# Kernel tuning notes

Measured on AMD Instinct MI355X. Metric: run time of the kernel, lower is better.

Reference implementation:

```python
import jax, jax.numpy as jnp
import numpy as np

N = 65536      # nodes in batched graph
E = 2097152    # edges (avg degree 32)
V = 1000       # chord vocabulary size
F_IN = 128     # chord feature dim
H = 256        # hidden_dim
OUT = 128      # out_dim
G = 256        # number of graphs in batch


def _gcn_layer(x, W, b, row, col, norm, n):
    # x: [n, f_in] -> [n, f_out]; PyG GCNConv: linear then normalized aggregation + bias
    x = x @ W
    msg = x[row] * norm[:, None]            # gather at source, scale by sym-norm
    return jax.ops.segment_sum(msg, col, num_segments=n) + b


def setup_inputs() -> dict:
    key = jax.random.key(0)
    ks = jax.random.split(key, 9)
    chord_feats = jax.random.normal(ks[0], (V, F_IN), jnp.float32)
    W1 = jax.random.normal(ks[1], (F_IN, H), jnp.float32) * 0.05
    b1 = jnp.zeros((H,), jnp.float32)
    W2 = jax.random.normal(ks[2], (H, OUT), jnp.float32) * 0.05
    b2 = jnp.zeros((OUT,), jnp.float32)
    edge_attr = jax.random.uniform(ks[3], (E,), jnp.float32)          # positive edge weights
    node_indices = jax.random.randint(ks[4], (N,), 0, V, jnp.int64)
    edge_index = jax.random.randint(ks[5], (2, E), 0, N, jnp.int64)
    batch_index = jnp.sort(jax.random.randint(ks[6], (N,), 0, G, jnp.int64))
    return {"chord_feats": chord_feats, "W1": W1, "b1": b1, "W2": W2, "b2": b2,
            "edge_attr": edge_attr, "node_indices": node_indices,
            "edge_index": edge_index, "batch_index": batch_index}


def reference(chord_feats, W1, b1, W2, b2, edge_attr, node_indices, edge_index, batch_index):
    loops = jnp.arange(N, dtype=edge_index.dtype)
    row = jnp.concatenate([edge_index[0], loops])   # source
    col = jnp.concatenate([edge_index[1], loops])   # target
    ew = jnp.concatenate([edge_attr, jnp.ones((N,), edge_attr.dtype)])  # self-loop weight 1
    # symmetric GCN normalization: D^-1/2 A D^-1/2
    deg = jax.ops.segment_sum(ew, col, num_segments=N)
    dis = jnp.where(deg > 0, jax.lax.rsqrt(jnp.maximum(deg, 1e-30)), 0.0)
    norm = dis[row] * ew * dis[col]

    x = chord_feats[node_indices]                   # [N, F_IN]
    x = jax.nn.relu(_gcn_layer(x, W1, b1, row, col, norm, N))
    x = jax.nn.relu(_gcn_layer(x, W2, b2, row, col, norm, N))

    # global_mean_pool over batch_index
    sums = jax.ops.segment_sum(x, batch_index, num_segments=G)
    counts = jax.ops.segment_sum(jnp.ones((N,), x.dtype), batch_index, num_segments=G)
    return sums / jnp.maximum(counts, 1.0)[:, None]
```

## Files before the change

kernel.cpp:

```cpp
#include <hip/hip_runtime.h>
#include <hip/hip_fp16.h>
#include <math.h>

constexpr int N_NODES = 65536;
constexpr int N_EDGES = 2097152;
constexpr int F_IN    = 128;
constexpr int H_DIM   = 256;
constexpr int O_DIM   = 128;
constexpr int N_GRAPH = 256;
constexpr int V_SIZE  = 1000;

constexpr int EPB  = 8192;
constexpr int NBLK = N_EDGES / EPB;
constexpr float FXP = 16777216.0f;

typedef _Float16 half8 __attribute__((ext_vector_type(8)));
typedef float floatx4 __attribute__((ext_vector_type(4)));


__global__ void k_init(float* __restrict__ pool, const int* __restrict__ batch,
                       float* __restrict__ cntf, const float* __restrict__ cf,
                       const float* __restrict__ W1, __half* __restrict__ cfW1,
                       const float* __restrict__ W2, _Float16* __restrict__ W2T) {
    __shared__ float xs[8 * F_IN];
    int i = blockIdx.x * blockDim.x + threadIdx.x;
    if (i < N_GRAPH * O_DIM) pool[i] = 0.0f;
    if (blockIdx.x == 0) {
        int g = threadIdx.x;
        int lo = 0, hi = N_NODES;
        while (lo < hi) { int m = (lo + hi) >> 1; if (batch[m] < g) lo = m + 1; else hi = m; }
        int start = lo;
        lo = 0; hi = N_NODES;
        while (lo < hi) { int m = (lo + hi) >> 1; if (batch[m] <= g) lo = m + 1; else hi = m; }
        cntf[g] = (float)(lo - start);
    }
    if (blockIdx.x < V_SIZE / 8) {
        int rb = blockIdx.x * 8;
        int t  = threadIdx.x;
        #pragma unroll
        for (int p = 0; p < 4; ++p) {
            int idx = p * 256 + t;
            int r = idx >> 7, k = idx & 127;
            xs[idx] = cf[(size_t)(rb + r) * F_IN + k];
        }
        __syncthreads();
        float acc[8] = {};
        for (int k = 0; k < F_IN; ++k) {
            float w = W1[k * H_DIM + t];
            #pragma unroll
            for (int j = 0; j < 8; ++j) acc[j] += xs[j * F_IN + k] * w;
        }
        #pragma unroll
        for (int j = 0; j < 8; ++j)
            cfW1[(size_t)(rb + j) * H_DIM + t] = __float2half(acc[j]);
    }
    if (blockIdx.x >= 128) {
        int idx = (blockIdx.x - 128) * 256 + threadIdx.x;
        int nn = idx >> 8, kk = idx & 255;
        W2T[idx] = (_Float16)W2[kk * O_DIM + nn];
    }
}


__global__ void k_hist(const int* __restrict__ col, int* __restrict__ hist) {
    __shared__ int h[256];
    int t = threadIdx.x;
    h[t] = 0;
    __syncthreads();
    int base = blockIdx.x * EPB;
    #pragma unroll
    for (int i = 0; i < EPB / 256; ++i)
        atomicAdd(&h[col[base + i * 256 + t] >> 8], 1);
    __syncthreads();
    hist[t * NBLK + blockIdx.x] = h[t];
}


__global__ void k_scan1(const int* __restrict__ in, int* __restrict__ out,
                        int* __restrict__ bsum) {
    __shared__ int s[256];
    int tid = threadIdx.x;
    int i = blockIdx.x * 256 + tid;
    int v = in[i];
    s[tid] = v;
    __syncthreads();
    for (int d = 1; d < 256; d <<= 1) {
        int t = (tid >= d) ? s[tid - d] : 0;
        __syncthreads();
        s[tid] += t;
        __syncthreads();
    }
    out[i] = s[tid] - v;
    if (tid == 255) bsum[blockIdx.x] = s[255];
}

__global__ void k_scan2(int* __restrict__ bsum) {
    __shared__ int s[256];
    int tid = threadIdx.x;
    int v = bsum[tid];
    s[tid] = v;
    __syncthreads();
    for (int d = 1; d < 256; d <<= 1) {
        int t = (tid >= d) ? s[tid - d] : 0;
        __syncthreads();
        s[tid] += t;
        __syncthreads();
    }
    bsum[tid] = s[tid] - v;
}


__global__ void k_part(const int* __restrict__ row, const int* __restrict__ col,
                       const float* __restrict__ ew, const int* __restrict__ nidx,
                       const int* __restrict__ hoffs, const int* __restrict__ bsum,
                       int2* __restrict__ part) {
    __shared__ int cur[256];
    int t = threadIdx.x;
    cur[t] = hoffs[t * NBLK + blockIdx.x] + bsum[t];
    __syncthreads();
    int base = blockIdx.x * EPB;
    for (int i = 0; i < EPB / 256; ++i) {
        int e = base + i * 256 + t;
        int r = row[e], c = col[e];
        unsigned hw = (unsigned)__half_as_ushort(__float2half(ew[e]));
        int vb = nidx[r];
        int slot = atomicAdd(&cur[c >> 8], 1);
        int2 rec;
        rec.x = (r << 16) | ((c & 255) << 8) | (vb >> 2);
        rec.y = (int)(((unsigned)(vb & 3) << 16) | hw);
        part[slot] = rec;
    }
}


__global__ void k_build1(const int* __restrict__ hoffs, const int* __restrict__ bsum,
                         const int2* __restrict__ part, float* __restrict__ dis,
                         int* __restrict__ offs) {
    __shared__ unsigned long long dc[256];
    __shared__ int sc[256];
    int t = threadIdx.x;
    int bucket = blockIdx.x;
    dc[t] = 0ULL;
    __syncthreads();
    int start = hoffs[bucket * NBLK] + bsum[bucket];
    int end   = (bucket == 255) ? N_EDGES : (hoffs[(bucket + 1) * NBLK] + bsum[bucket + 1]);
    for (int j = start + t; j < end; j += 256) {
        int2 rec = part[j];
        int dst = (rec.x >> 8) & 255;
        float w = __half2float(__ushort_as_half((unsigned short)(rec.y & 0xFFFF)));
        atomicAdd(&dc[dst], (1ULL << 40) |
                  (unsigned long long)(unsigned)(w * FXP + 0.5f));
    }
    __syncthreads();
    unsigned long long v = dc[t];
    float deg = 1.0f + (float)(v & 0xFFFFFFFFFFULL) * (1.0f / FXP);
    dis[bucket * 256 + t] = 1.0f / sqrtf(deg);
    int cnt = (int)(v >> 40);
    sc[t] = cnt;
    __syncthreads();
    for (int d = 1; d < 256; d <<= 1) {
        int x = (t >= d) ? sc[t - d] : 0;
        __syncthreads();
        sc[t] += x;
        __syncthreads();
    }
    offs[bucket * 256 + t] = start + sc[t] - cnt;
    if (bucket == 255 && t == 255) offs[N_NODES] = N_EDGES;
}


__global__ void k_build2(const int* __restrict__ hoffs, const int* __restrict__ bsum,
                         const int2* __restrict__ part, const float* __restrict__ dis,
                         const int* __restrict__ offs, int2* __restrict__ csr) {
    __shared__ int cur[256];
    int t = threadIdx.x;
    int bucket = blockIdx.x;
    cur[t] = offs[bucket * 256 + t];
    __syncthreads();
    int start = hoffs[bucket * NBLK] + bsum[bucket];
    int end   = (bucket == 255) ? N_EDGES : (hoffs[(bucket + 1) * NBLK] + bsum[bucket + 1]);
    for (int j = start + t; j < end; j += 256) {
        int2 rec = part[j];
        int dst = (rec.x >> 8) & 255;
        unsigned src = ((unsigned)rec.x) >> 16;
        int vb = ((rec.x & 255) << 2) | ((rec.y >> 16) & 3);
        float w = __half2float(__ushort_as_half((unsigned short)(rec.y & 0xFFFF)));
        float nm = dis[src] * w;
        int slot = atomicAdd(&cur[dst], 1);
        int2 e;
        e.x = (int)((src << 10) | (unsigned)vb);
        e.y = __float_as_int(nm);
        csr[slot] = e;
    }
}


__global__ void k_agg1(const int2* __restrict__ cfW1, const int* __restrict__ nidx,
                       const float* __restrict__ dis, const int* __restrict__ offs,
                       const int2* __restrict__ csr, const float4* __restrict__ b1f4,
                       int2* __restrict__ h1) {
    int wave = threadIdx.x >> 6;
    int lane = threadIdx.x & 63;
    int c = blockIdx.x * 4 + wave;
    float d = dis[c];
    int2 sp = cfW1[(size_t)nidx[c] * 64 + lane];
    float2 sa = __half22float2(*(__half2*)&sp.x);
    float2 sb = __half22float2(*(__half2*)&sp.y);
    float4 esum = {0.f, 0.f, 0.f, 0.f};
    int a0 = offs[c], a1 = offs[c + 1];
    int s = a0;
    for (; s + 8 <= a1; s += 8) {
        int sb_i = __builtin_amdgcn_readfirstlane(s);
        int2 e[8];
        #pragma unroll
        for (int u = 0; u < 8; ++u) e[u] = csr[sb_i + u];
        int2 v[8];
        #pragma unroll
        for (int u = 0; u < 8; ++u)
            v[u] = cfW1[(size_t)(e[u].x & 1023) * 64 + lane];
        #pragma unroll
        for (int u = 0; u < 8; ++u) {
            float n = __int_as_float(e[u].y);
            float2 va = __half22float2(*(__half2*)&v[u].x);
            float2 vb = __half22float2(*(__half2*)&v[u].y);
            esum.x += va.x * n; esum.y += va.y * n;
            esum.z += vb.x * n; esum.w += vb.y * n;
        }
    }
    for (; s < a1; ++s) {
        int sb_i = __builtin_amdgcn_readfirstlane(s);
        int2 e0 = csr[sb_i];
        int2 v0 = cfW1[(size_t)(e0.x & 1023) * 64 + lane];
        float n = __int_as_float(e0.y);
        float2 va = __half22float2(*(__half2*)&v0.x);
        float2 vb = __half22float2(*(__half2*)&v0.y);
        esum.x += va.x * n; esum.y += va.y * n;
        esum.z += vb.x * n; esum.w += vb.y * n;
    }
    float4 bb = b1f4[lane];
    float dd = d * d;
    float r0 = bb.x + sa.x * dd + d * esum.x;
    float r1 = bb.y + sa.y * dd + d * esum.y;
    float r2 = bb.z + sb.x * dd + d * esum.z;
    float r3 = bb.w + sb.y * dd + d * esum.w;
    r0 = r0 > 0.f ? r0 : 0.f;  r1 = r1 > 0.f ? r1 : 0.f;
    r2 = r2 > 0.f ? r2 : 0.f;  r3 = r3 > 0.f ? r3 : 0.f;
    float2 p0 = {r0, r1}, p1 = {r2, r3};
    __half2 ha = __float22half2_rn(p0);
    __half2 hb = __float22half2_rn(p1);
    int2 outv;
    outv.x = *(int*)&ha;
    outv.y = *(int*)&hb;
    h1[(size_t)c * 64 + lane] = outv;
}


__global__ void k_gemm2(const _Float16* __restrict__ h1, const _Float16* __restrict__ W2T,
                        __half* __restrict__ xw2h) {
    int wave = threadIdx.x >> 6;
    int lane = threadIdx.x & 63;
    int quad = lane >> 4;
    int n    = lane & 15;
    int tm   = blockIdx.x * 4 + wave;
    const _Float16* arow = h1 + (size_t)(tm * 16 + n) * H_DIM;
    half8 a[8];
    #pragma unroll
    for (int kt = 0; kt < 8; ++kt)
        a[kt] = *(const half8*)(arow + kt * 32 + quad * 8);
    #pragma unroll
    for (int nt = 0; nt < 8; ++nt) {
        floatx4 acc = {0.f, 0.f, 0.f, 0.f};
        const _Float16* brow = W2T + (size_t)(nt * 16 + n) * H_DIM;
        #pragma unroll
        for (int kt = 0; kt < 8; ++kt) {
            half8 b = *(const half8*)(brow + kt * 32 + quad * 8);
            acc = __builtin_amdgcn_mfma_f32_16x16x32_f16(a[kt], b, acc, 0, 0, 0);
        }
        #pragma unroll
        for (int r = 0; r < 4; ++r) {
            int rowi = tm * 16 + quad * 4 + r;
            xw2h[(size_t)rowi * O_DIM + nt * 16 + n] = __float2half(acc[r]);
        }
    }
}


__global__ void k_agg2_pool(const __half2* __restrict__ xw2h, const float* __restrict__ b2,
                            const float* __restrict__ dis, const int* __restrict__ offs,
                            const int2* __restrict__ csr, const int* __restrict__ batch,
                            float* __restrict__ pool) {
    __shared__ float2 red[4][64];
    __shared__ int bgs[4];
    int wave = threadIdx.x >> 6;
    int lane = threadIdx.x & 63;
    int c = blockIdx.x * 4 + wave;
    float d = dis[c];
    float2 self = __half22float2(xw2h[(size_t)c * 64 + lane]);
    float2 bb = ((const float2*)b2)[lane];
    float2 esum = {0.f, 0.f};
    int s0 = offs[c], s1 = offs[c + 1];
    int s = s0;
    for (; s + 8 <= s1; s += 8) {
        int sb_i = __builtin_amdgcn_readfirstlane(s);
        int2 e[8];
        #pragma unroll
        for (int u = 0; u < 8; ++u) e[u] = csr[sb_i + u];
        float2 v[8];
        #pragma unroll
        for (int u = 0; u < 8; ++u)
            v[u] = __half22float2(xw2h[(size_t)(e[u].x >> 10) * 64 + lane]);
        #pragma unroll
        for (int u = 0; u < 8; ++u) {
            float n = __int_as_float(e[u].y);
            esum.x += v[u].x * n; esum.y += v[u].y * n;
        }
    }
    for (; s < s1; ++s) {
        int sb_i = __builtin_amdgcn_readfirstlane(s);
        int2 e0 = csr[sb_i];
        float2 v0 = __half22float2(xw2h[(size_t)(e0.x >> 10) * 64 + lane]);
        float n0 = __int_as_float(e0.y);
        esum.x += v0.x * n0; esum.y += v0.y * n0;
    }
    float dd = d * d;
    float2 acc;
    acc.x = bb.x + self.x * dd + d * esum.x;
    acc.y = bb.y + self.y * dd + d * esum.y;
    acc.x = acc.x > 0.0f ? acc.x : 0.0f;
    acc.y = acc.y > 0.0f ? acc.y : 0.0f;
    red[wave][lane] = acc;
    if (lane == 0) bgs[wave] = batch[c];
    __syncthreads();
    if (wave == 0) {
        float2 a = red[0][lane];
        int cg = bgs[0];
        #pragma unroll
        for (int w = 1; w < 4; ++w) {
            int g = bgs[w];
            float2 r = red[w][lane];
            if (g == cg) { a.x += r.x; a.y += r.y; }
            else {
                atomicAdd(&pool[cg * O_DIM + 2 * lane], a.x);
                atomicAdd(&pool[cg * O_DIM + 2 * lane + 1], a.y);
                a = r; cg = g;
            }
        }
        atomicAdd(&pool[cg * O_DIM + 2 * lane], a.x);
        atomicAdd(&pool[cg * O_DIM + 2 * lane + 1], a.y);
    }
}

__global__ void k_final(const float* __restrict__ pool, const float* __restrict__ cnt,
                        float* __restrict__ out) {
    int t = blockIdx.x * blockDim.x + threadIdx.x;
    if (t < N_GRAPH * O_DIM) {
        int g = t / O_DIM;
        out[t] = pool[t] / fmaxf(cnt[g], 1.0f);
    }
}


extern "C" void kernel_launch(void* const* d_in, const int* in_sizes, int n_in,
                              void* d_out, int out_size, void* d_ws, size_t ws_size,
                              hipStream_t stream) {
    const float* cf   = (const float*)d_in[0];
    const float* W1   = (const float*)d_in[1];
    const float* b1   = (const float*)d_in[2];
    const float* W2   = (const float*)d_in[3];
    const float* b2   = (const float*)d_in[4];
    const float* ew   = (const float*)d_in[5];
    const int*   nidx = (const int*)d_in[6];
    const int*   eidx = (const int*)d_in[7];
    const int*   bidx = (const int*)d_in[8];
    float* out = (float*)d_out;

    const int* row = eidx;
    const int* col = eidx + N_EDGES;

    char* ws = (char*)d_ws;
    size_t off = 0;
    int*   hist  = (int*)  (ws + off); off += (size_t)N_NODES * 4;
    int*   hoffs = (int*)  (ws + off); off += (size_t)N_NODES * 4;
    int*   bsum  = (int*)  (ws + off); off += 4096;
    float* dis   = (float*)(ws + off); off += (size_t)N_NODES * 4;
    int*   offs  = (int*)  (ws + off); off += (size_t)(N_NODES + 16) * 4;
    int2*  csr   = (int2*) (ws + off); off += (size_t)N_EDGES * 8;
    float* pool  = (float*)(ws + off); off += (size_t)(N_GRAPH * O_DIM + N_GRAPH) * 4;
    __half* cfW1 = (__half*)(ws + off); off += (size_t)V_SIZE * H_DIM * 2;
    _Float16* W2T = (_Float16*)(ws + off); off += (size_t)O_DIM * H_DIM * 2;
    off = (off + 255) & ~(size_t)255;
    int2*  part  = (int2*) (ws + off); off += (size_t)N_EDGES * 8;
    __half* h1   = (__half*)(ws + off);
    __half* xw2h = (__half*)part;
    float* cntf  = pool + N_GRAPH * O_DIM;

    k_init<<<256, 256, 0, stream>>>(pool, bidx, cntf, cf, W1, cfW1, W2, W2T);
    k_hist<<<NBLK, 256, 0, stream>>>(col, hist);
    k_scan1<<<256, 256, 0, stream>>>(hist, hoffs, bsum);
    k_scan2<<<1, 256, 0, stream>>>(bsum);

    k_part<<<NBLK, 256, 0, stream>>>(row, col, ew, nidx, hoffs, bsum, part);
    k_build1<<<256, 256, 0, stream>>>(hoffs, bsum, part, dis, offs);
    k_build2<<<256, 256, 0, stream>>>(hoffs, bsum, part, dis, offs, csr);

    k_agg1<<<N_NODES / 4, 256, 0, stream>>>((const int2*)cfW1, nidx, dis, offs, csr,
                                            (const float4*)b1, (int2*)h1);

    k_gemm2<<<N_NODES / 64, 256, 0, stream>>>((const _Float16*)h1, W2T, xw2h);
    k_agg2_pool<<<N_NODES / 4, 256, 0, stream>>>((const __half2*)xw2h, b2, dis, offs, csr,
                                                 bidx, pool);

    k_final<<<(N_GRAPH * O_DIM + 255) / 256, 256, 0, stream>>>(pool, cntf, out);
}
```

Before: 348.7 us.

## Widen gathers to 16-byte loads and split each wave across multiple edges

Both aggregation kernels now have each lane gather 8 halves (int4) instead of 2 or 4, so one wave covers a feature row with 16 or 32 lanes and processes several edges at once. Partial sums are combined with cross-lane xor shuffles before the bias, ReLU and store. The goal is fewer, wider memory transactions per gathered row and more edges in flight per wave, cutting load instruction count in these latency-bound gather loops. It adds shuffle reductions and tail handling (odd-start alignment, padded lanes) that idle lanes on low-degree nodes.

```diff
diff --git a/kernel.cpp b/kernel.cpp
--- a/kernel.cpp
+++ b/kernel.cpp
@@ -194,64 +194,103 @@
     }
 }
 
-
-__global__ void k_agg1(const int2* __restrict__ cfW1, const int* __restrict__ nidx,
+__device__ __forceinline__ void acc8(float* e, int4 v, float n) {
+    float2 f0 = __half22float2(*(__half2*)&v.x);
+    float2 f1 = __half22float2(*(__half2*)&v.y);
+    float2 f2 = __half22float2(*(__half2*)&v.z);
+    float2 f3 = __half22float2(*(__half2*)&v.w);
+    e[0] += f0.x * n; e[1] += f0.y * n;
+    e[2] += f1.x * n; e[3] += f1.y * n;
+    e[4] += f2.x * n; e[5] += f2.y * n;
+    e[6] += f3.x * n; e[7] += f3.y * n;
+}
+
+
+__global__ void k_agg1(const int4* __restrict__ cfW1, const int* __restrict__ nidx,
                        const float* __restrict__ dis, const int* __restrict__ offs,
                        const int2* __restrict__ csr, const float4* __restrict__ b1f4,
-                       int2* __restrict__ h1) {
+                       int4* __restrict__ h1) {
     int wave = threadIdx.x >> 6;
     int lane = threadIdx.x & 63;
+    int g    = lane >> 5;
+    int sl   = lane & 31;
     int c = blockIdx.x * 4 + wave;
     float d = dis[c];
-    int2 sp = cfW1[(size_t)nidx[c] * 64 + lane];
-    float2 sa = __half22float2(*(__half2*)&sp.x);
-    float2 sb = __half22float2(*(__half2*)&sp.y);
-    float4 esum = {0.f, 0.f, 0.f, 0.f};
+    int4 sp = cfW1[(size_t)nidx[c] * 32 + sl];
+    float esum[8] = {0.f, 0.f, 0.f, 0.f, 0.f, 0.f, 0.f, 0.f};
     int a0 = offs[c], a1 = offs[c + 1];
     int s = a0;
+    if (s < a1 && (s & 1)) {
+        int sb = __builtin_amdgcn_readfirstlane(s);
+        int2 e0 = csr[sb];
+        int4 v0 = cfW1[(size_t)(e0.x & 1023) * 32 + sl];
+        float n = (g == 0) ? __int_as_float(e0.y) : 0.0f;
+        acc8(esum, v0, n);
+        ++s;
+    }
     for (; s + 8 <= a1; s += 8) {
-        int sb_i = __builtin_amdgcn_readfirstlane(s);
-        int2 e[8];
-        #pragma unroll
-        for (int u = 0; u < 8; ++u) e[u] = csr[sb_i + u];
-        int2 v[8];
-        #pragma unroll
-        for (int u = 0; u < 8; ++u)
-            v[u] = cfW1[(size_t)(e[u].x & 1023) * 64 + lane];
-        #pragma unroll
-        for (int u = 0; u < 8; ++u) {
-            float n = __int_as_float(e[u].y);
-            float2 va = __half22float2(*(__half2*)&v[u].x);
-            float2 vb = __half22float2(*(__half2*)&v[u].y);
-            esum.x += va.x * n; esum.y += va.y * n;
-            esum.z += vb.x * n; esum.w += vb.y * n;
-        }
-    }
-    for (; s < a1; ++s) {
-        int sb_i = __builtin_amdgcn_readfirstlane(s);
-        int2 e0 = csr[sb_i];
-        int2 v0 = cfW1[(size_t)(e0.x & 1023) * 64 + lane];
-        float n = __int_as_float(e0.y);
-        float2 va = __half22float2(*(__half2*)&v0.x);
-        float2 vb = __half22float2(*(__half2*)&v0.y);
-        esum.x += va.x * n; esum.y += va.y * n;
-        esum.z += vb.x * n; esum.w += vb.y * n;
-    }
-    float4 bb = b1f4[lane];
+        int sb = __builtin_amdgcn_readfirstlane(s);
+        int4 ee[4];
+        #pragma unroll
+        for (int u = 0; u < 4; ++u) ee[u] = *(const int4*)(csr + sb + 2 * u);
+        int4 v[4]; float n[4];
+        #pragma unroll
+        for (int u = 0; u < 4; ++u) {
+            int ex = g ? ee[u].z : ee[u].x;
+            int ey = g ? ee[u].w : ee[u].y;
+            n[u] = __int_as_float(ey);
+            v[u] = cfW1[(size_t)(ex & 1023) * 32 + sl];
+        }
+        #pragma unroll
+        for (int u = 0; u < 4; ++u) acc8(esum, v[u], n[u]);
+    }
+    for (; s + 2 <= a1; s += 2) {
+        int sb = __builtin_amdgcn_readfirstlane(s);
+        int4 ee = *(const int4*)(csr + sb);
+        int ex = g ? ee.z : ee.x;
+        int ey = g ? ee.w : ee.y;
+        int4 v0 = cfW1[(size_t)(ex & 1023) * 32 + sl];
+        acc8(esum, v0, __int_as_float(ey));
+    }
+    if (s < a1) {
+        int sb = __builtin_amdgcn_readfirstlane(s);
+        int2 e0 = csr[sb];
+        int4 v0 = cfW1[(size_t)(e0.x & 1023) * 32 + sl];
+        float n = (g == 0) ? __int_as_float(e0.y) : 0.0f;
+        acc8(esum, v0, n);
+    }
+    #pragma unroll
+    for (int k = 0; k < 8; ++k) esum[k] += __shfl_xor(esum[k], 32, 64);
+
     float dd = d * d;
-    float r0 = bb.x + sa.x * dd + d * esum.x;
-    float r1 = bb.y + sa.y * dd + d * esum.y;
-    float r2 = bb.z + sb.x * dd + d * esum.z;
-    float r3 = bb.w + sb.y * dd + d * esum.w;
-    r0 = r0 > 0.f ? r0 : 0.f;  r1 = r1 > 0.f ? r1 : 0.f;
-    r2 = r2 > 0.f ? r2 : 0.f;  r3 = r3 > 0.f ? r3 : 0.f;
-    float2 p0 = {r0, r1}, p1 = {r2, r3};
-    __half2 ha = __float22half2_rn(p0);
-    __half2 hb = __float22half2_rn(p1);
-    int2 outv;
-    outv.x = *(int*)&ha;
-    outv.y = *(int*)&hb;
-    h1[(size_t)c * 64 + lane] = outv;
+    float2 s0 = __half22float2(*(__half2*)&sp.x);
+    float2 s1 = __half22float2(*(__half2*)&sp.y);
+    float2 s2 = __half22float2(*(__half2*)&sp.z);
+    float2 s3 = __half22float2(*(__half2*)&sp.w);
+    float4 bb0 = b1f4[2 * sl];
+    float4 bb1 = b1f4[2 * sl + 1];
+    float r[8];
+    r[0] = bb0.x + s0.x * dd + d * esum[0];
+    r[1] = bb0.y + s0.y * dd + d * esum[1];
+    r[2] = bb0.z + s1.x * dd + d * esum[2];
+    r[3] = bb0.w + s1.y * dd + d * esum[3];
+    r[4] = bb1.x + s2.x * dd + d * esum[4];
+    r[5] = bb1.y + s2.y * dd + d * esum[5];
+    r[6] = bb1.z + s3.x * dd + d * esum[6];
+    r[7] = bb1.w + s3.y * dd + d * esum[7];
+    #pragma unroll
+    for (int k = 0; k < 8; ++k) r[k] = r[k] > 0.f ? r[k] : 0.f;
+    float2 p0 = {r[0], r[1]}, p1 = {r[2], r[3]}, p2 = {r[4], r[5]}, p3 = {r[6], r[7]};
+    __half2 h0 = __float22half2_rn(p0);
+    __half2 h1v = __float22half2_rn(p1);
+    __half2 h2 = __float22half2_rn(p2);
+    __half2 h3 = __float22half2_rn(p3);
+    int4 outv;
+    outv.x = *(int*)&h0;
+    outv.y = *(int*)&h1v;
+    outv.z = *(int*)&h2;
+    outv.w = *(int*)&h3;
+    if (lane < 32) h1[(size_t)c * 32 + sl] = outv;
 }
 
 
@@ -285,59 +324,89 @@
 }
 
 
-__global__ void k_agg2_pool(const __half2* __restrict__ xw2h, const float* __restrict__ b2,
+__global__ void k_agg2_pool(const int4* __restrict__ xw2h, const float* __restrict__ b2,
                             const float* __restrict__ dis, const int* __restrict__ offs,
                             const int2* __restrict__ csr, const int* __restrict__ batch,
                             float* __restrict__ pool) {
-    __shared__ float2 red[4][64];
+    __shared__ float red[4][128];
     __shared__ int bgs[4];
     int wave = threadIdx.x >> 6;
     int lane = threadIdx.x & 63;
+    int grp  = lane >> 4;
+    int sl   = lane & 15;
     int c = blockIdx.x * 4 + wave;
     float d = dis[c];
-    float2 self = __half22float2(xw2h[(size_t)c * 64 + lane]);
-    float2 bb = ((const float2*)b2)[lane];
-    float2 esum = {0.f, 0.f};
+    int4 sp = xw2h[(size_t)c * 16 + sl];
+    float esum[8] = {0.f, 0.f, 0.f, 0.f, 0.f, 0.f, 0.f, 0.f};
     int s0 = offs[c], s1 = offs[c + 1];
     int s = s0;
-    for (; s + 8 <= s1; s += 8) {
-        int sb_i = __builtin_amdgcn_readfirstlane(s);
-        int2 e[8];
-        #pragma unroll
-        for (int u = 0; u < 8; ++u) e[u] = csr[sb_i + u];
-        float2 v[8];
-        #pragma unroll
-        for (int u = 0; u < 8; ++u)
-            v[u] = __half22float2(xw2h[(size_t)(e[u].x >> 10) * 64 + lane]);
-        #pragma unroll
-        for (int u = 0; u < 8; ++u) {
-            float n = __int_as_float(e[u].y);
-            esum.x += v[u].x * n; esum.y += v[u].y * n;
-        }
-    }
-    for (; s < s1; ++s) {
-        int sb_i = __builtin_amdgcn_readfirstlane(s);
-        int2 e0 = csr[sb_i];
-        float2 v0 = __half22float2(xw2h[(size_t)(e0.x >> 10) * 64 + lane]);
-        float n0 = __int_as_float(e0.y);
-        esum.x += v0.x * n0; esum.y += v0.y * n0;
+    for (; s + 16 <= s1; s += 16) {
+        int sb = __builtin_amdgcn_readfirstlane(s);
+        int2 e[4];
+        #pragma unroll
+        for (int u = 0; u < 4; ++u) e[u] = csr[sb + 4 * u + grp];
+        int4 v[4];
+        #pragma unroll
+        for (int u = 0; u < 4; ++u)
+            v[u] = xw2h[(size_t)(((unsigned)e[u].x) >> 10) * 16 + sl];
+        #pragma unroll
+        for (int u = 0; u < 4; ++u) acc8(esum, v[u], __int_as_float(e[u].y));
+    }
+    for (; s + 4 <= s1; s += 4) {
+        int sb = __builtin_amdgcn_readfirstlane(s);
+        int2 e0 = csr[sb + grp];
+        int4 v0 = xw2h[(size_t)(((unsigned)e0.x) >> 10) * 16 + sl];
+        acc8(esum, v0, __int_as_float(e0.y));
+    }
+    if (s < s1) {
+        int sb = __builtin_amdgcn_readfirstlane(s);
+        int idx = sb + grp;
+        int idc = idx < s1 ? idx : s1 - 1;
+        int2 e0 = csr[idc];
+        int4 v0 = xw2h[(size_t)(((unsigned)e0.x) >> 10) * 16 + sl];
+        float n = (idx < s1) ? __int_as_float(e0.y) : 0.0f;
+        acc8(esum, v0, n);
+    }
+    #pragma unroll
+    for (int k = 0; k < 8; ++k) {
+        esum[k] += __shfl_xor(esum[k], 16, 64);
+        esum[k] += __shfl_xor(esum[k], 32, 64);
     }
     float dd = d * d;
-    float2 acc;
-    acc.x = bb.x + self.x * dd + d * esum.x;
-    acc.y = bb.y + self.y * dd + d * esum.y;
-    acc.x = acc.x > 0.0f ? acc.x : 0.0f;
-    acc.y = acc.y > 0.0f ? acc.y : 0.0f;
-    red[wave][lane] = acc;
+    float2 f0 = __half22float2(*(__half2*)&sp.x);
+    float2 f1 = __half22float2(*(__half2*)&sp.y);
+    float2 f2 = __half22float2(*(__half2*)&sp.z);
+    float2 f3 = __half22float2(*(__half2*)&sp.w);
+    float4 bb0 = ((const float4*)b2)[2 * sl];
+    float4 bb1 = ((const float4*)b2)[2 * sl + 1];
+    float acc[8];
+    acc[0] = bb0.x + f0.x * dd + d * esum[0];
+    acc[1] = bb0.y + f0.y * dd + d * esum[1];
+    acc[2] = bb0.z + f1.x * dd + d * esum[2];
+    acc[3] = bb0.w + f1.y * dd + d * esum[3];
+    acc[4] = bb1.x + f2.x * dd + d * esum[4];
+    acc[5] = bb1.y + f2.y * dd + d * esum[5];
+    acc[6] = bb1.z + f3.x * dd + d * esum[6];
+    acc[7] = bb1.w + f3.y * dd + d * esum[7];
+    #pragma unroll
+    for (int k = 0; k < 8; ++k) acc[k] = acc[k] > 0.f ? acc[k] : 0.f;
+    if (grp == 0) {
+        #pragma unroll
+        for (int k = 0; k < 8; ++k) red[wave][8 * sl + k] = acc[k];
+    }
     if (lane == 0) bgs[wave] = batch[c];
     __syncthreads();
     if (wave == 0) {
-        float2 a = red[0][lane];
+        float2 a;
+        a.x = red[0][2 * lane];
+        a.y = red[0][2 * lane + 1];
         int cg = bgs[0];
         #pragma unroll
         for (int w = 1; w < 4; ++w) {
             int g = bgs[w];
-            float2 r = red[w][lane];
+            float2 r;
+            r.x = red[w][2 * lane];
+            r.y = red[w][2 * lane + 1];
             if (g == cg) { a.x += r.x; a.y += r.y; }
             else {
                 atomicAdd(&pool[cg * O_DIM + 2 * lane], a.x);
@@ -403,11 +472,11 @@
     k_build1<<<256, 256, 0, stream>>>(hoffs, bsum, part, dis, offs);
     k_build2<<<256, 256, 0, stream>>>(hoffs, bsum, part, dis, offs, csr);
 
-    k_agg1<<<N_NODES / 4, 256, 0, stream>>>((const int2*)cfW1, nidx, dis, offs, csr,
-                                            (const float4*)b1, (int2*)h1);
+    k_agg1<<<N_NODES / 4, 256, 0, stream>>>((const int4*)cfW1, nidx, dis, offs, csr,
+                                            (const float4*)b1, (int4*)h1);
 
     k_gemm2<<<N_NODES / 64, 256, 0, stream>>>((const _Float16*)h1, W2T, xw2h);
-    k_agg2_pool<<<N_NODES / 4, 256, 0, stream>>>((const __half2*)xw2h, b2, dis, offs, csr,
+    k_agg2_pool<<<N_NODES / 4, 256, 0, stream>>>((const int4*)xw2h, b2, dis, offs, csr,
                                                  bidx, pool);
 
     k_final<<<(N_GRAPH * O_DIM + 255) / 256, 256, 0, stream>>>(pool, cntf, out);
```

Result: faster. 331.5 us (-4.9%).
